# Kernel tuning notes

Measured on AMD Instinct MI355X. Metric: run time of the kernel, lower is better.

Reference implementation:

```python
import jax, jax.numpy as jnp
import numpy as np

H_PARAM = 3.0   # filtering strength h
TWS = 5         # template window size
SWS = 11        # search window size


def _shift_stack(x, window_size):
    # [N,C,H,W] -> [N,C,H,W,window_size**2] of circularly shifted copies.
    # Shift order matches the torch module: outer loop x_shift, inner y_shift,
    # roll shifts=(y_shift, x_shift) on dims (H, W).
    r = window_size // 2
    return jnp.stack(
        [jnp.roll(x, (ys, xs), axis=(2, 3))
         for xs in range(-r, r + 1) for ys in range(-r, r + 1)],
        axis=-1,
    )


def _box_filter(x, window_size):
    # Circular box-sum over H,W dims. The torch double roll loop is separable,
    # so do it as two 1-D roll sums (10 rolls instead of 25 for tws=5).
    r = window_size // 2
    s = x
    acc = x
    for k in range(1, r + 1):
        acc = acc + jnp.roll(s, k, axis=3) + jnp.roll(s, -k, axis=3)
    s2 = acc
    for k in range(1, r + 1):
        acc = acc + jnp.roll(s2, k, axis=2) + jnp.roll(s2, -k, axis=2)
    return acc


def setup_inputs() -> dict:
    key = jax.random.key(0)
    x = jax.random.uniform(key, (2, 3, 512, 512), dtype=jnp.float32)
    return {"x": x}


def reference(x):
    # luminance (RGB input: C == 3)
    xc = jnp.clip(x, 0.0, 1.0)
    y = 0.299 * xc[:, :1] + 0.587 * xc[:, 1:2] + 0.114 * xc[:, 2:3]  # [N,1,H,W]

    x_stack = _shift_stack(x, SWS)  # [N,3,H,W,sws^2]
    y_stack = _shift_stack(y, SWS)  # [N,1,H,W,sws^2]

    d2 = _box_filter((y[..., None] - y_stack) ** 2, TWS)  # [N,1,H,W,sws^2]
    distances = jnp.sqrt(d2)
    weights = jnp.exp(-distances / H_PARAM)                # [N,1,H,W,sws^2]

    denoised = (weights * x_stack).sum(axis=-1) / weights.sum(axis=-1)
    return jnp.clip(denoised, 0.0, 1.0)
```

## Files before the change

### kernel.cpp

```cpp
#include <hip/hip_runtime.h>
#include <math.h>


#define H_IMG 512
#define W_IMG 512
#define MASK  511
#define HWSZ  (H_IMG * W_IMG)
#define TILE  32
#define HALO  7
#define XD    46
#define YSTR  48
#define HSTR  44
#define VSTR  44

typedef _Float16 h2 __attribute__((ext_vector_type(2)));
typedef float f32x2 __attribute__((ext_vector_type(2)));

__device__ __forceinline__ float fdot2(h2 a, h2 b, float c) {
#if __has_builtin(__builtin_amdgcn_fdot2)
    return __builtin_amdgcn_fdot2(a, b, c, false);
#else
    return c + (float)a.x * (float)b.x + (float)a.y * (float)b.y;
#endif
}

__device__ __forceinline__ float fast_exp2(float x) {
#if __has_builtin(__builtin_amdgcn_exp2f)
    return __builtin_amdgcn_exp2f(x);
#else
    return __expf(x * 0.6931471805599453f);
#endif
}

#define K2C   0.23126321070979063f
#define N2K2 -0.46252642141958126f

__global__ __launch_bounds__(512, 2)
void nlm_kernel(const float* __restrict__ x, float* __restrict__ out) {
    __shared__ float4   ldsX[XD * XD];
    __shared__ float    ldsYf[XD * YSTR];
    __shared__ unsigned ldsY2[XD * YSTR];
    __shared__ float    ldsH[XD * HSTR];
    __shared__ float    ldsV[42 * VSTR];

    const int n  = blockIdx.z;
    const int ti = blockIdx.y * TILE;
    const int tj = blockIdx.x * TILE;
    const int tx = threadIdx.x;
    const int ty = threadIdx.y;
    const int tz = threadIdx.z;
    const int tid = tz * 256 + ty * 32 + tx;

    const float* xb = x + (size_t)n * 3 * HWSZ;

    for (int e = tid; e < XD * XD; e += 512) {
        int r = e / XD, c = e - r * XD;
        int gi = (ti + r - HALO) & MASK;
        int gj = (tj + c - HALO) & MASK;
        size_t o = (size_t)gi * W_IMG + gj;
        ldsX[e] = make_float4(xb[o], xb[o + HWSZ], xb[o + 2 * HWSZ], 0.f);
    }
    __syncthreads();

    for (int e = tid; e < XD * 47; e += 512) {
        int r = e / 47, c = e - r * 47;
        int cs = (c == 46) ? 45 : c;
        float4 v = ldsX[r * XD + cs];
        float rr = fminf(fmaxf(v.x, 0.f), 1.f);
        float gg = fminf(fmaxf(v.y, 0.f), 1.f);
        float bb = fminf(fmaxf(v.z, 0.f), 1.f);
        ldsYf[r * YSTR + c] = 0.299f * rr + 0.587f * gg + 0.114f * bb;
    }
    __syncthreads();

    for (int e = tid; e < XD * XD; e += 512) {
        int r = e / XD, c = e - r * XD;
        h2 p;
        p.x = (_Float16)ldsYf[r * YSTR + c];
        p.y = (_Float16)ldsYf[r * YSTR + c + 1];
        ldsY2[r * YSTR + c] = __builtin_bit_cast(unsigned, p);
    }
    __syncthreads();

    for (int e = tid; e < XD * 42; e += 512) {
        int r = e / 42, c = e - r * 42;
        h2 a  = __builtin_bit_cast(h2, ldsY2[r * YSTR + c]);
        h2 b  = __builtin_bit_cast(h2, ldsY2[r * YSTR + c + 2]);
        h2 cc = __builtin_bit_cast(h2, ldsY2[r * YSTR + c + 4]);
        float x0 = (float)a.x, x1 = (float)a.y;
        float x2 = (float)b.x, x3 = (float)b.y;
        float x4 = (float)cc.x;
        ldsH[r * HSTR + c] = x0*x0 + x1*x1 + x2*x2 + x3*x3 + x4*x4;
    }
    __syncthreads();

    for (int e = tid; e < 42 * 42; e += 512) {
        int r = e / 42, c = e - r * 42;
        const float* hp = &ldsH[r * HSTR + c];
        float s = ((hp[0] + hp[HSTR]) + (hp[2*HSTR] + hp[3*HSTR])) + hp[4*HSTR];
        ldsV[r * VSTR + c] = K2C * s;
    }
    __syncthreads();

    const int jl = tx + HALO;
    const int il = ty * 4 + HALO;

    h2 cyP[8][3];
    float Vc[4];
    #pragma unroll
    for (int t = 0; t < 8; ++t) {
        int base = (il - 2 + t) * YSTR + (jl - 2);
        cyP[t][0] = __builtin_bit_cast(h2, ldsY2[base]);
        cyP[t][1] = __builtin_bit_cast(h2, ldsY2[base + 2]);
        h2 z = __builtin_bit_cast(h2, ldsY2[base + 4]);
        z.y = (_Float16)0.f;
        cyP[t][2] = z;
    }
    #pragma unroll
    for (int o = 0; o < 4; ++o)
        Vc[o] = ldsV[(il - 2 + o) * VSTR + (jl - 2)];

    f32x2 acc01[4];
    float num2[4], den[4];
    #pragma unroll
    for (int o = 0; o < 4; ++o) {
        acc01[o] = (f32x2){0.f, 0.f};
        num2[o] = 0.f; den[o] = 0.f;
    }

    const int xs_lo = tz ? 1 : -5;
    const int xs_hi = tz ? 5 : 0;

    #pragma unroll 1
    for (int xs = xs_lo; xs <= xs_hi; ++xs) {
        const int jc  = jl - xs - 2;
        const int xjc = jl - xs;

        unsigned swU[8][3];
        float  Wr[4];
        float  xw0[4], xw1[4], xw2[4];

        #pragma unroll
        for (int t = 0; t < 8; ++t) {
            int base = (il - 7 + t) * YSTR + jc;
            swU[t][0] = ldsY2[base];
            swU[t][1] = ldsY2[base + 2];
            swU[t][2] = ldsY2[base + 4];
        }
        #pragma unroll
        for (int t = 0; t < 4; ++t) {
            Wr[t] = ldsV[(il - 7 + t) * VSTR + jc];
            float4 xv = ldsX[(il - 5 + t) * XD + xjc];
            xw0[t] = xv.x; xw1[t] = xv.y; xw2[t] = xv.z;
        }

        float pd2[4];
        float px0, px1, px2;

        #pragma unroll
        for (int k = 0; k <= 10; ++k) {
            unsigned nu0, nu1, nu2; float nWv, nx0, nx1, nx2;
            if (k < 10) {
                const int nr = il + k + 1;
                int base = nr * YSTR + jc;
                nu0 = ldsY2[base];
                nu1 = ldsY2[base + 2];
                nu2 = ldsY2[base + 4];
                nWv = ldsV[(il + k - 3) * VSTR + jc];
                float4 xv = ldsX[(il + k - 1) * XD + xjc];
                nx0 = xv.x; nx1 = xv.y; nx2 = xv.z;
            }

            float s[8];
            #pragma unroll
            for (int t = 0; t < 8; ++t) {
                const int m = (t + k) & 7;
                s[t] = fdot2(cyP[t][0], __builtin_bit_cast(h2, swU[m][0]),
                       fdot2(cyP[t][1], __builtin_bit_cast(h2, swU[m][1]),
                       fdot2(cyP[t][2], __builtin_bit_cast(h2, swU[m][2]), 0.f)));
            }

            float S0 = ((s[0] + s[1]) + (s[2] + s[3])) + s[4];
            float S1 = S0 - s[0] + s[5];
            float S2 = S1 - s[1] + s[6];
            float S3 = S2 - s[2] + s[7];

            float d2a[4];
            d2a[0] = fmaf(N2K2, S0, Vc[0] + Wr[k & 3]);
            d2a[1] = fmaf(N2K2, S1, Vc[1] + Wr[(k + 1) & 3]);
            d2a[2] = fmaf(N2K2, S2, Vc[2] + Wr[(k + 2) & 3]);
            d2a[3] = fmaf(N2K2, S3, Vc[3] + Wr[(k + 3) & 3]);

            if (k > 0) {
                #pragma unroll
                for (int o = 0; o < 4; ++o) {
                    int sl = (k - 1 + o) & 3;
                    float v0 = (o == 0) ? px0 : xw0[sl];
                    float v1 = (o == 0) ? px1 : xw1[sl];
                    float v2 = (o == 0) ? px2 : xw2[sl];
                    float sd = __builtin_amdgcn_sqrtf(__builtin_fabsf(pd2[o]));
                    float w  = fast_exp2(-sd);
                    f32x2 bw = {w, w};
                    f32x2 xv01 = {v0, v1};
                    acc01[o] = __builtin_elementwise_fma(bw, xv01, acc01[o]);
                    num2[o] = fmaf(w, v2, num2[o]);
                    den[o] += w;
                }
            }

            #pragma unroll
            for (int o = 0; o < 4; ++o) pd2[o] = d2a[o];
            if (k < 10) {
                asm volatile("" : "+v"(nu0), "+v"(nu1), "+v"(nu2),
                                  "+v"(nWv), "+v"(nx0), "+v"(nx1), "+v"(nx2));
                px0 = xw0[k & 3]; px1 = xw1[k & 3]; px2 = xw2[k & 3];
                swU[k & 7][0] = nu0;
                swU[k & 7][1] = nu1;
                swU[k & 7][2] = nu2;
                Wr[k & 3] = nWv;
                xw0[k & 3] = nx0; xw1[k & 3] = nx1; xw2[k & 3] = nx2;
            }
        }

        #pragma unroll
        for (int o = 0; o < 4; ++o) {
            int sl = (10 + o) & 3;
            float sd = __builtin_amdgcn_sqrtf(__builtin_fabsf(pd2[o]));
            float w  = fast_exp2(-sd);
            f32x2 bw = {w, w};
            f32x2 xv01 = {xw0[sl], xw1[sl]};
            acc01[o] = __builtin_elementwise_fma(bw, xv01, acc01[o]);
            num2[o] = fmaf(w, xw2[sl], num2[o]);
            den[o] += w;
        }
    }

    __syncthreads();
    float4* red = (float4*)ldsX;
    const int t = ty * 32 + tx;
    if (tz == 1) {
        #pragma unroll
        for (int o = 0; o < 4; ++o)
            red[o * 256 + t] = make_float4(acc01[o].x, acc01[o].y, num2[o], den[o]);
    }
    __syncthreads();

    if (tz == 0) {
        float* ob = out + (size_t)n * 3 * HWSZ;
        #pragma unroll
        for (int o = 0; o < 4; ++o) {
            float4 p = red[o * 256 + t];
            float n0 = acc01[o].x + p.x;
            float n1 = acc01[o].y + p.y;
            float n2 = num2[o] + p.z;
            float dn = den[o] + p.w;
            int gi = ti + ty * 4 + o;
            int gj = tj + tx;
            size_t off = (size_t)gi * W_IMG + gj;
            float inv = __builtin_amdgcn_rcpf(dn);
            float v0 = fminf(fmaxf(n0 * inv, 0.f), 1.f);
            float v1 = fminf(fmaxf(n1 * inv, 0.f), 1.f);
            float v2 = fminf(fmaxf(n2 * inv, 0.f), 1.f);
            ob[off]            = v0;
            ob[off + HWSZ]     = v1;
            ob[off + 2 * HWSZ] = v2;
        }
    }
}

extern "C" void kernel_launch(void* const* d_in, const int* in_sizes, int n_in,
                              void* d_out, int out_size, void* d_ws, size_t ws_size,
                              hipStream_t stream) {
    const float* x = (const float*)d_in[0];
    float* out = (float*)d_out;
    dim3 grid(W_IMG / TILE, H_IMG / TILE, 2);
    dim3 block(32, 8, 2);
    nlm_kernel<<<grid, block, 0, stream>>>(x, out);
}
```

Measured before the change: 101.8 us.

## Split search-window columns across three thread slices instead of two

The block grows from 512 to 768 threads by adding a third z-slice. The 11 horizontal search offsets are now split 4/4/3 across the slices instead of 6/5, so each thread runs a shorter serial loop and more waves are resident to hide latency. Partial sums from two slices are merged through shared memory before the final normalisation. In exchange, the launch bound of 768 threads with 2 blocks per CU tightens the per-thread register budget, which may cause spills, and the reduction adds extra LDS traffic.

```diff
diff --git a/kernel.cpp b/kernel.cpp
--- a/kernel.cpp
+++ b/kernel.cpp
@@ -12,6 +12,7 @@
 #define YSTR  48
 #define HSTR  44
 #define VSTR  44
+#define NTHR  768
 
 typedef _Float16 h2 __attribute__((ext_vector_type(2)));
 typedef float f32x2 __attribute__((ext_vector_type(2)));
@@ -35,7 +36,7 @@
 #define K2C   0.23126321070979063f
 #define N2K2 -0.46252642141958126f
 
-__global__ __launch_bounds__(512, 2)
+__global__ __launch_bounds__(NTHR, 2)
 void nlm_kernel(const float* __restrict__ x, float* __restrict__ out) {
     __shared__ float4   ldsX[XD * XD];
     __shared__ float    ldsYf[XD * YSTR];
@@ -53,7 +54,7 @@
 
     const float* xb = x + (size_t)n * 3 * HWSZ;
 
-    for (int e = tid; e < XD * XD; e += 512) {
+    for (int e = tid; e < XD * XD; e += NTHR) {
         int r = e / XD, c = e - r * XD;
         int gi = (ti + r - HALO) & MASK;
         int gj = (tj + c - HALO) & MASK;
@@ -62,7 +63,7 @@
     }
     __syncthreads();
 
-    for (int e = tid; e < XD * 47; e += 512) {
+    for (int e = tid; e < XD * 47; e += NTHR) {
         int r = e / 47, c = e - r * 47;
         int cs = (c == 46) ? 45 : c;
         float4 v = ldsX[r * XD + cs];
@@ -73,7 +74,7 @@
     }
     __syncthreads();
 
-    for (int e = tid; e < XD * XD; e += 512) {
+    for (int e = tid; e < XD * XD; e += NTHR) {
         int r = e / XD, c = e - r * XD;
         h2 p;
         p.x = (_Float16)ldsYf[r * YSTR + c];
@@ -82,7 +83,7 @@
     }
     __syncthreads();
 
-    for (int e = tid; e < XD * 42; e += 512) {
+    for (int e = tid; e < XD * 42; e += NTHR) {
         int r = e / 42, c = e - r * 42;
         h2 a  = __builtin_bit_cast(h2, ldsY2[r * YSTR + c]);
         h2 b  = __builtin_bit_cast(h2, ldsY2[r * YSTR + c + 2]);
@@ -94,7 +95,7 @@
     }
     __syncthreads();
 
-    for (int e = tid; e < 42 * 42; e += 512) {
+    for (int e = tid; e < 42 * 42; e += NTHR) {
         int r = e / 42, c = e - r * 42;
         const float* hp = &ldsH[r * HSTR + c];
         float s = ((hp[0] + hp[HSTR]) + (hp[2*HSTR] + hp[3*HSTR])) + hp[4*HSTR];
@@ -128,8 +129,8 @@
         num2[o] = 0.f; den[o] = 0.f;
     }
 
-    const int xs_lo = tz ? 1 : -5;
-    const int xs_hi = tz ? 5 : 0;
+    const int xs_lo = -5 + tz * 4;
+    const int xs_hi = (tz == 2) ? 5 : (xs_lo + 3);
 
     #pragma unroll 1
     for (int xs = xs_lo; xs <= xs_hi; ++xs) {
@@ -238,10 +239,11 @@
     __syncthreads();
     float4* red = (float4*)ldsX;
     const int t = ty * 32 + tx;
-    if (tz == 1) {
+    if (tz != 0) {
         #pragma unroll
         for (int o = 0; o < 4; ++o)
-            red[o * 256 + t] = make_float4(acc01[o].x, acc01[o].y, num2[o], den[o]);
+            red[((tz - 1) * 4 + o) * 256 + t] =
+                make_float4(acc01[o].x, acc01[o].y, num2[o], den[o]);
     }
     __syncthreads();
 
@@ -249,11 +251,12 @@
         float* ob = out + (size_t)n * 3 * HWSZ;
         #pragma unroll
         for (int o = 0; o < 4; ++o) {
-            float4 p = red[o * 256 + t];
-            float n0 = acc01[o].x + p.x;
-            float n1 = acc01[o].y + p.y;
-            float n2 = num2[o] + p.z;
-            float dn = den[o] + p.w;
+            float4 p1 = red[o * 256 + t];
+            float4 p2 = red[(4 + o) * 256 + t];
+            float n0 = acc01[o].x + p1.x + p2.x;
+            float n1 = acc01[o].y + p1.y + p2.y;
+            float n2 = num2[o] + p1.z + p2.z;
+            float dn = den[o] + p1.w + p2.w;
             int gi = ti + ty * 4 + o;
             int gj = tj + tx;
             size_t off = (size_t)gi * W_IMG + gj;
@@ -274,6 +277,6 @@
     const float* x = (const float*)d_in[0];
     float* out = (float*)d_out;
     dim3 grid(W_IMG / TILE, H_IMG / TILE, 2);
-    dim3 block(32, 8, 2);
+    dim3 block(32, 8, 3);
     nlm_kernel<<<grid, block, 0, stream>>>(x, out);
 }
```

Result: faster. 99.61 us (-2.1%).
